# Optimization experiments

Measured on AMD Instinct MI355X. Metric: run time of the kernel, lower is better.

The kernel has to match this reference:

```python
import jax, jax.numpy as jnp
import numpy as np

LRELU_ALPHA = 0.2       # LeakyReLU slope (alpha arg of GraphAttentionLayer)
NEG_INF = -9e15         # zero_vec value from the torch code
N1, N2, N3 = 3000, 2500, 2500
IN_F, OUT_F, HEADS = 128, 64, 2


def setup_inputs() -> dict:
    key = jax.random.key(0)
    ks = jax.random.split(key, 13)
    N = N1 + N2 + N3
    h = jax.random.normal(ks[0], (N, IN_F), jnp.float32)
    A1  = jax.random.randint(ks[1],  (N1, N1), 0, 2, jnp.int32)
    A2  = jax.random.randint(ks[2],  (N2, N2), 0, 2, jnp.int32)
    A3  = jax.random.randint(ks[3],  (N3, N3), 0, 2, jnp.int32)
    A12 = jax.random.randint(ks[4],  (N1, N2), 0, 2, jnp.int32)
    A13 = jax.random.randint(ks[5],  (N1, N3), 0, 2, jnp.int32)
    A23 = jax.random.randint(ks[6],  (N2, N3), 0, 2, jnp.int32)
    A21 = jax.random.randint(ks[7],  (N2, N1), 0, 2, jnp.int32)
    A31 = jax.random.randint(ks[8],  (N3, N1), 0, 2, jnp.int32)
    A32 = jax.random.randint(ks[9],  (N3, N2), 0, 2, jnp.int32)
    # per-head GAT parameters (xavier-ish scale)
    Ws = jax.random.normal(ks[10], (HEADS, IN_F, OUT_F), jnp.float32) * 0.12
    a_param = jax.random.normal(ks[11], (HEADS, 2 * OUT_F, 1), jnp.float32) * 0.12
    return dict(h=h, A1=A1, A2=A2, A3=A3, A12=A12, A13=A13, A23=A23,
                A21=A21, A31=A31, A32=A32, Ws=Ws, a_param=a_param)


def reference(h, A1, A2, A3, A12, A13, A23, A21, A31, A32, Ws, a_param):
    n1, n2, n3 = A1.shape[0], A2.shape[0], A3.shape[0]
    # The 9 block assignments in the torch forward tile the full NxN matrix,
    # so they are equivalent to one block-structured mask.
    mask = jnp.block([[A1,  A12, A13],
                      [A21, A2,  A23],
                      [A31, A32, A3]]) > 0          # [N, N] bool

    Wh = jnp.einsum('nf,hfo->hno', h, Ws)           # [H, N, O]
    a1 = a_param[:, :OUT_F, 0]                      # [H, O]
    a2 = a_param[:, OUT_F:, 0]                      # [H, O]
    Wh1 = jnp.einsum('hno,ho->hn', Wh, a1)          # [H, N]
    Wh2 = jnp.einsum('hno,ho->hn', Wh, a2)          # [H, N]
    e = jax.nn.leaky_relu(Wh1[:, :, None] + Wh2[:, None, :], LRELU_ALPHA)  # [H,N,N]
    att = jax.nn.softmax(jnp.where(mask[None], e, NEG_INF), axis=-1)
    # dropout is identity in eval mode
    mid = jnp.einsum('hij,hjo->hio', att, Wh)       # [H, N, O]
    out = jax.nn.elu(mid)                           # concat=True -> elu
    x2 = out.transpose(1, 0, 2).reshape(h.shape[0], -1)  # [N, H*O] head concat

    x3 = jax.nn.log_softmax(x2[n1 + n2:], axis=1)   # group-3 nodes
    x4 = jax.nn.log_softmax(x2[:n1], axis=1)        # group-1 nodes
    x5 = jax.nn.log_softmax(x2[n1:n1 + n2], axis=1) # group-2 nodes
    return (x3, x4, x5)
```

## Files before the change

### kernel.cpp

```cpp
#include <hip/hip_runtime.h>
#include <hip/hip_bf16.h>


#define CN1 3000
#define CN2 2500
#define CN3 2500
#define NTOT 8000
#define INF_ 128
#define OUTF 64
#define LOG2E 1.44269504088896340736f
#define ALPHA 0.2f

typedef __attribute__((ext_vector_type(4))) float f32x4;
typedef __attribute__((ext_vector_type(8))) short short8;
union B16x8 { int4 i4; short8 s8; unsigned int u[4]; };

#if defined(__has_builtin)
#if __has_builtin(__builtin_amdgcn_exp2f)
#define EXP2F(x) __builtin_amdgcn_exp2f(x)
#endif
#endif
#ifndef EXP2F
#define EXP2F(x) exp2f(x)
#endif

__device__ inline float wave_sum(float v) {
  for (int d = 32; d; d >>= 1) v += __shfl_xor(v, d, 64);
  return v;
}

__device__ inline unsigned int pack2_bf16(float a, float b) {
  unsigned ua = __float_as_uint(a);
  ua = (ua + 0x7FFFu + ((ua >> 16) & 1u)) >> 16;
  unsigned ub = __float_as_uint(b);
  ub = (ub + 0x7FFFu + ((ub >> 16) & 1u)) & 0xFFFF0000u;
  return ub | ua;
}

__global__ void k_wh(const float* __restrict__ hv, const float* __restrict__ Wsv,
                     const float* __restrict__ ap,
                     float* __restrict__ Whf,
                     float* __restrict__ Wh1s,
                     float* __restrict__ Wh2s) {
  const int t = threadIdx.x;
  const int o = t & 63;
  const int n = blockIdx.x * 2 + (t >> 6);
  const float* hrow = hv + n * INF_;
  const float* Ws0 = Wsv + o;
  const float* Ws1 = Wsv + INF_ * OUTF + o;
  float a0a = 0.f, a0b = 0.f, a1a = 0.f, a1b = 0.f;
#pragma unroll 8
  for (int f = 0; f < INF_; f += 2) {
    float h0 = hrow[f], h1 = hrow[f + 1];
    a0a += h0 * Ws0[f * OUTF];
    a0b += h1 * Ws0[(f + 1) * OUTF];
    a1a += h0 * Ws1[f * OUTF];
    a1b += h1 * Ws1[(f + 1) * OUTF];
  }
  float acc0 = a0a + a0b, acc1 = a1a + a1b;
  Whf[(0 * NTOT + n) * OUTF + o] = acc0;
  Whf[(1 * NTOT + n) * OUTF + o] = acc1;
  float s10 = wave_sum(acc0 * ap[o]);
  float s20 = wave_sum(acc0 * ap[OUTF + o]);
  float s11 = wave_sum(acc1 * ap[2 * OUTF + o]);
  float s21 = wave_sum(acc1 * ap[3 * OUTF + o]);
  if (o == 0) {
    Wh1s[n] = s10 * LOG2E;        Wh2s[n] = s20 * LOG2E;
    Wh1s[NTOT + n] = s11 * LOG2E; Wh2s[NTOT + n] = s21 * LOG2E;
  }
}

__global__ void k_m2(const float* __restrict__ Wh2s, float* __restrict__ M2s) {
  const int hd = blockIdx.x;
  float mx = -1e30f;
  for (int i = threadIdx.x; i < NTOT; i += 256)
    mx = fmaxf(mx, Wh2s[hd * NTOT + i]);
  for (int d = 32; d; d >>= 1) mx = fmaxf(mx, __shfl_xor(mx, d, 64));
  __shared__ float red[4];
  if ((threadIdx.x & 63) == 0) red[threadIdx.x >> 6] = mx;
  __syncthreads();
  if (threadIdx.x == 0)
    M2s[hd] = fmaxf(fmaxf(red[0], red[1]), fmaxf(red[2], red[3]));
}

__global__ void k_bpack(const float* __restrict__ Whf, int4* __restrict__ WhB) {
  const int gid = blockIdx.x * 256 + threadIdx.x;
  const int lane = gid & 63;
  const int c = (gid >> 6) & 3;
  const int t = (gid >> 8) % 250;
  const int hd = gid / 64000;
  const int jb = t * 32 + (lane >> 4) * 8;
  const int col = c * 16 + (lane & 15);
  const float* src = Whf + (hd * NTOT + jb) * OUTF + col;
  B16x8 out;
#pragma unroll
  for (int e2 = 0; e2 < 4; ++e2)
    out.u[e2] = pack2_bf16(src[(2 * e2) * OUTF], src[(2 * e2 + 1) * OUTF]);
  WhB[gid] = out.i4;
}

__global__ __launch_bounds__(128, 2)
void k_attn_mfma(const int* __restrict__ A1,  const int* __restrict__ A12, const int* __restrict__ A13,
                 const int* __restrict__ A21, const int* __restrict__ A2,  const int* __restrict__ A23,
                 const int* __restrict__ A31, const int* __restrict__ A32, const int* __restrict__ A3,
                 const float* __restrict__ Wh1s, const float* __restrict__ Wh2s,
                 const float* __restrict__ M2s, const int4* __restrict__ WhB,
                 float* __restrict__ partAcc,
                 float* __restrict__ partS)
{
  const int widx = threadIdx.x >> 6;
  const int lane = threadIdx.x & 63;
  const int m = lane & 15;
  const int g = lane >> 4;
  const int kb = g * 8;
  const int rowblk = blockIdx.x * 2 + widx;
  const int i = rowblk * 16 + m;
  const int jy = blockIdx.y, njy = gridDim.y;
  const int t0 = (250 * jy) / njy, t1 = (250 * (jy + 1)) / njy;

  const int *p0, *p1, *p2;
  if (i < CN1)            { p0 = A1  + i * CN1;          p1 = A12 + i * CN2;          p2 = A13 + i * CN3; }
  else if (i < CN1 + CN2) { int r = i - CN1;       p0 = A21 + r * CN1; p1 = A2  + r * CN2; p2 = A23 + r * CN3; }
  else                    { int r = i - CN1 - CN2; p0 = A31 + r * CN1; p1 = A32 + r * CN2; p2 = A3  + r * CN3; }

  const float w1s0 = Wh1s[i],        w1s1 = Wh1s[NTOT + i];
  const float y0 = w1s0 + M2s[0],    y1 = w1s1 + M2s[1];
  const float ci0 = fmaxf(y0, ALPHA * y0), ci1 = fmaxf(y1, ALPHA * y1);
  const float a1c0 = w1s0 - ci0, b1c0 = ALPHA * w1s0 - ci0;
  const float a1c1 = w1s1 - ci1, b1c1 = ALPHA * w1s1 - ci1;
  const float* wh2_0 = Wh2s;
  const float* wh2_1 = Wh2s + NTOT;

  f32x4 a0_0 = {0.f,0.f,0.f,0.f}, a0_1 = a0_0, a0_2 = a0_0, a0_3 = a0_0;
  f32x4 a1_0 = a0_0, a1_1 = a0_0, a1_2 = a0_0, a1_3 = a0_0;
  float sp0 = 0.f, sp1 = 0.f;

  auto load_mask = [&](int t, int4& ma, int4& mb) {
    int j8 = t * 32 + kb;
    if (j8 >= CN1 + CN2) {
      const int4* q = (const int4*)(p2 + (j8 - CN1 - CN2));
      ma = q[0]; mb = q[1];
    } else if (j8 >= CN1) {
      if (j8 + 8 <= CN1 + CN2) {
        const int4* q = (const int4*)(p1 + (j8 - CN1));
        ma = q[0]; mb = q[1];
      } else {
        int v[8];
#pragma unroll
        for (int e = 0; e < 8; ++e) {
          int je = j8 + e;
          v[e] = (je < CN1 + CN2) ? p1[je - CN1] : p2[je - CN1 - CN2];
        }
        ma = make_int4(v[0], v[1], v[2], v[3]);
        mb = make_int4(v[4], v[5], v[6], v[7]);
      }
    } else {
      const int4* q = (const int4*)(p0 + j8);
      ma = q[0]; mb = q[1];
    }
  };

  struct Frags { int4 f0[4], f1[4]; float4 w0a, w0b, w1a, w1b; };
  auto load_frags = [&](int t, Frags& F) {
    const int4* bp0 = WhB + t * 256 + lane;
    const int4* bp1 = WhB + (250 + t) * 256 + lane;
#pragma unroll
    for (int c = 0; c < 4; ++c) { F.f0[c] = bp0[c * 64]; F.f1[c] = bp1[c * 64]; }
    const float* w0 = wh2_0 + t * 32 + kb;
    const float* w1 = wh2_1 + t * 32 + kb;
    F.w0a = *(const float4*)w0; F.w0b = *(const float4*)(w0 + 4);
    F.w1a = *(const float4*)w1; F.w1b = *(const float4*)(w1 + 4);
  };

  auto compute = [&](const int4& ma, const int4& mb, const Frags& F) {
    const int   mv[8] = {ma.x, ma.y, ma.z, ma.w, mb.x, mb.y, mb.z, mb.w};
    const float w0v[8] = {F.w0a.x, F.w0a.y, F.w0a.z, F.w0a.w, F.w0b.x, F.w0b.y, F.w0b.z, F.w0b.w};
    const float w1v[8] = {F.w1a.x, F.w1a.y, F.w1a.z, F.w1a.w, F.w1b.x, F.w1b.y, F.w1b.z, F.w1b.w};
    float q0[8], q1[8];
#pragma unroll
    for (int e = 0; e < 8; ++e) {
      bool on = (mv[e] > 0);
      float xa0 = a1c0 + w0v[e];
      float xb0 = fmaf(ALPHA, w0v[e], b1c0);
      float p0e = EXP2F(fmaxf(xa0, xb0));
      q0[e] = on ? p0e : 0.f;
      float xa1 = a1c1 + w1v[e];
      float xb1 = fmaf(ALPHA, w1v[e], b1c1);
      float p1e = EXP2F(fmaxf(xa1, xb1));
      q1[e] = on ? p1e : 0.f;
    }
    sp0 += ((q0[0] + q0[1]) + (q0[2] + q0[3])) + ((q0[4] + q0[5]) + (q0[6] + q0[7]));
    sp1 += ((q1[0] + q1[1]) + (q1[2] + q1[3])) + ((q1[4] + q1[5]) + (q1[6] + q1[7]));
    B16x8 af0, af1;
#pragma unroll
    for (int e2 = 0; e2 < 4; ++e2) {
      af0.u[e2] = pack2_bf16(q0[2 * e2], q0[2 * e2 + 1]);
      af1.u[e2] = pack2_bf16(q1[2 * e2], q1[2 * e2 + 1]);
    }
    B16x8 b;
    b.i4 = F.f0[0]; a0_0 = __builtin_amdgcn_mfma_f32_16x16x32_bf16(af0.s8, b.s8, a0_0, 0, 0, 0);
    b.i4 = F.f0[1]; a0_1 = __builtin_amdgcn_mfma_f32_16x16x32_bf16(af0.s8, b.s8, a0_1, 0, 0, 0);
    b.i4 = F.f0[2]; a0_2 = __builtin_amdgcn_mfma_f32_16x16x32_bf16(af0.s8, b.s8, a0_2, 0, 0, 0);
    b.i4 = F.f0[3]; a0_3 = __builtin_amdgcn_mfma_f32_16x16x32_bf16(af0.s8, b.s8, a0_3, 0, 0, 0);
    b.i4 = F.f1[0]; a1_0 = __builtin_amdgcn_mfma_f32_16x16x32_bf16(af1.s8, b.s8, a1_0, 0, 0, 0);
    b.i4 = F.f1[1]; a1_1 = __builtin_amdgcn_mfma_f32_16x16x32_bf16(af1.s8, b.s8, a1_1, 0, 0, 0);
    b.i4 = F.f1[2]; a1_2 = __builtin_amdgcn_mfma_f32_16x16x32_bf16(af1.s8, b.s8, a1_2, 0, 0, 0);
    b.i4 = F.f1[3]; a1_3 = __builtin_amdgcn_mfma_f32_16x16x32_bf16(af1.s8, b.s8, a1_3, 0, 0, 0);
  };

  int4 ma0, mb0, ma1, mb1, ma2, mb2, ma3, mb3;
  Frags Fc, Fn;
  load_mask(t0, ma0, mb0);
  load_mask(min(t0 + 1, t1 - 1), ma1, mb1);
  load_mask(min(t0 + 2, t1 - 1), ma2, mb2);
  load_frags(t0, Fc);
  for (int t = t0; t < t1; ++t) {
    load_frags(min(t + 1, t1 - 1), Fn);
    load_mask(min(t + 3, t1 - 1), ma3, mb3);
    compute(ma0, mb0, Fc);
    ma0 = ma1; mb0 = mb1; ma1 = ma2; mb1 = mb2; ma2 = ma3; mb2 = mb3;
    Fc = Fn;
  }

  sp0 += __shfl_xor(sp0, 16, 64); sp0 += __shfl_xor(sp0, 32, 64);
  sp1 += __shfl_xor(sp1, 16, 64); sp1 += __shfl_xor(sp1, 32, 64);
  const int base0 = (jy * 2 + 0) * NTOT + rowblk * 16;
  const int base1 = (jy * 2 + 1) * NTOT + rowblk * 16;
  if (lane < 16) {
    partS[base0 + lane] = sp0;
    partS[base1 + lane] = sp1;
  }

  float* o0 = partAcc + base0 * OUTF;
  float* o1 = partAcc + base1 * OUTF;
#pragma unroll
  for (int q = 0; q < 4; ++q) {
    const int row = g * 4 + q;
    o0[row * OUTF +      m] = a0_0[q];
    o0[row * OUTF + 16 + m] = a0_1[q];
    o0[row * OUTF + 32 + m] = a0_2[q];
    o0[row * OUTF + 48 + m] = a0_3[q];
    o1[row * OUTF +      m] = a1_0[q];
    o1[row * OUTF + 16 + m] = a1_1[q];
    o1[row * OUTF + 32 + m] = a1_2[q];
    o1[row * OUTF + 48 + m] = a1_3[q];
  }
}

__global__ void k_final(const float* __restrict__ partAcc, const float* __restrict__ partS,
                        int njy, float* __restrict__ out) {
  const int wave = threadIdx.x >> 6, lane = threadIdx.x & 63;
  const int n = blockIdx.x * 4 + wave;
  float x[2];
#pragma unroll
  for (int hd = 0; hd < 2; ++hd) {
    float a = 0.f, s = 0.f;
    for (int jy = 0; jy < njy; ++jy) {
      a += partAcc[((jy * 2 + hd) * NTOT + n) * OUTF + lane];
      s += partS[(jy * 2 + hd) * NTOT + n];
    }
    float mid = a / s;
    x[hd] = mid > 0.f ? mid : (__expf(mid) - 1.f);
  }
  float mx = fmaxf(x[0], x[1]);
  for (int d = 32; d; d >>= 1) mx = fmaxf(mx, __shfl_xor(mx, d, 64));
  float se = __expf(x[0] - mx) + __expf(x[1] - mx);
  for (int d = 32; d; d >>= 1) se += __shfl_xor(se, d, 64);
  const float lse = mx + __logf(se);
  const int orow = (n >= CN1 + CN2) ? (n - CN1 - CN2) : (n + CN3);
  out[orow * 128 + lane]      = x[0] - lse;
  out[orow * 128 + 64 + lane] = x[1] - lse;
}

__global__ void k_sentinel(float* __restrict__ out, float v) {
  out[blockIdx.x * 256 + threadIdx.x] = v;
}

extern "C" void kernel_launch(void* const* d_in, const int* in_sizes, int n_in,
                              void* d_out, int out_size, void* d_ws, size_t ws_size,
                              hipStream_t stream) {
  float* outf = (float*)d_out;

  static const int EXP[12] = {1024000, 9000000, 6250000, 6250000, 7500000, 7500000,
                              6250000, 7500000, 7500000, 6250000, 16384, 256};
  bool exact = (n_in == 12);
  if (exact) for (int i = 0; i < 12; ++i) if (in_sizes[i] != EXP[i]) { exact = false; break; }

  const size_t FIXED = 64000 + 64000 + 256 + 2048000;
  int njy = 0;
  for (int cand = 4; cand >= 1; cand >>= 1) {
    size_t need = FIXED + (size_t)cand * 64000 +
                  ((size_t)(cand > 1 ? cand : 1)) * 4096000;
    if (ws_size >= need) { njy = cand; break; }
  }
  if (!exact || njy == 0) {
    k_sentinel<<<dim3(4000), dim3(256), 0, stream>>>(outf, -148.0f);
    return;
  }

  const float* h  = (const float*)d_in[0];
  const int* A1  = (const int*)d_in[1];
  const int* A2  = (const int*)d_in[2];
  const int* A3  = (const int*)d_in[3];
  const int* A12 = (const int*)d_in[4];
  const int* A13 = (const int*)d_in[5];
  const int* A23 = (const int*)d_in[6];
  const int* A21 = (const int*)d_in[7];
  const int* A31 = (const int*)d_in[8];
  const int* A32 = (const int*)d_in[9];
  const float* Ws = (const float*)d_in[10];
  const float* ap = (const float*)d_in[11];

  char* w = (char*)d_ws;
  float* Wh1s    = (float*)(w);
  float* Wh2s    = (float*)(w + 64000);
  float* M2s     = (float*)(w + 128000);
  int4*  WhB     = (int4*) (w + 128256);
  float* partS   = (float*)(w + 2176256);
  float* Whf     = (float*)(w + 2176256 + (size_t)njy * 64000);
  float* partAcc = Whf;

  k_wh       <<<dim3(4000),     dim3(128), 0, stream>>>(h, Ws, ap, Whf, Wh1s, Wh2s);
  k_m2       <<<dim3(2),        dim3(256), 0, stream>>>(Wh2s, M2s);
  k_bpack    <<<dim3(500),      dim3(256), 0, stream>>>(Whf, WhB);
  k_attn_mfma<<<dim3(250, njy), dim3(128), 0, stream>>>(A1, A12, A13, A21, A2, A23, A31, A32, A3,
                                                        Wh1s, Wh2s, M2s, WhB, partAcc, partS);
  k_final    <<<dim3(2000),     dim3(256), 0, stream>>>(partAcc, partS, njy, outf);
}
```

Measured before the change: 407.9 us.

## Pre-pack adjacency masks into bitmasks before the attention MFMA kernel

```diff
diff --git a/kernel.cpp b/kernel.cpp
--- a/kernel.cpp
+++ b/kernel.cpp
@@ -35,6 +35,31 @@
   unsigned ub = __float_as_uint(b);
   ub = (ub + 0x7FFFu + ((ub >> 16) & 1u)) & 0xFFFF0000u;
   return ub | ua;
+}
+
+__global__ __launch_bounds__(256)
+void k_pack(const int* __restrict__ A1,  const int* __restrict__ A12, const int* __restrict__ A13,
+            const int* __restrict__ A21, const int* __restrict__ A2,  const int* __restrict__ A23,
+            const int* __restrict__ A31, const int* __restrict__ A32, const int* __restrict__ A3,
+            unsigned int* __restrict__ packed) {
+  const int i = blockIdx.x * 4 + (threadIdx.x >> 6);
+  const int lane = threadIdx.x & 63;
+  const int *p0, *p1, *p2;
+  if (i < CN1)            { p0 = A1  + i * CN1;          p1 = A12 + i * CN2;          p2 = A13 + i * CN3; }
+  else if (i < CN1 + CN2) { int r = i - CN1;       p0 = A21 + r * CN1; p1 = A2  + r * CN2; p2 = A23 + r * CN3; }
+  else                    { int r = i - CN1 - CN2; p0 = A31 + r * CN1; p1 = A32 + r * CN2; p2 = A3  + r * CN3; }
+  unsigned int* pkrow = packed + (i >> 4) * 4000 + (i & 15);
+  for (int c = 0; c < 125; ++c) {
+    const int j = c * 64 + lane;
+    int mval = (j < CN1) ? p0[j]
+             : (j < CN1 + CN2) ? p1[j - CN1]
+                               : p2[j - CN1 - CN2];
+    unsigned long long bm = __ballot(mval > 0);
+    if (lane == 0) {
+      pkrow[(2 * c) * 16]     = (unsigned int)(bm & 0xffffffffull);
+      pkrow[(2 * c + 1) * 16] = (unsigned int)(bm >> 32);
+    }
+  }
 }
 
 __global__ void k_wh(const float* __restrict__ hv, const float* __restrict__ Wsv,
@@ -100,9 +125,7 @@
 }
 
 __global__ __launch_bounds__(128, 2)
-void k_attn_mfma(const int* __restrict__ A1,  const int* __restrict__ A12, const int* __restrict__ A13,
-                 const int* __restrict__ A21, const int* __restrict__ A2,  const int* __restrict__ A23,
-                 const int* __restrict__ A31, const int* __restrict__ A32, const int* __restrict__ A3,
+void k_attn_mfma(const unsigned int* __restrict__ packed,
                  const float* __restrict__ Wh1s, const float* __restrict__ Wh2s,
                  const float* __restrict__ M2s, const int4* __restrict__ WhB,
                  float* __restrict__ partAcc,
@@ -118,10 +141,7 @@
   const int jy = blockIdx.y, njy = gridDim.y;
   const int t0 = (250 * jy) / njy, t1 = (250 * (jy + 1)) / njy;
 
-  const int *p0, *p1, *p2;
-  if (i < CN1)            { p0 = A1  + i * CN1;          p1 = A12 + i * CN2;          p2 = A13 + i * CN3; }
-  else if (i < CN1 + CN2) { int r = i - CN1;       p0 = A21 + r * CN1; p1 = A2  + r * CN2; p2 = A23 + r * CN3; }
-  else                    { int r = i - CN1 - CN2; p0 = A31 + r * CN1; p1 = A32 + r * CN2; p2 = A3  + r * CN3; }
+  const unsigned int* pkb = packed + rowblk * 4000 + m;
 
   const float w1s0 = Wh1s[i],        w1s1 = Wh1s[NTOT + i];
   const float y0 = w1s0 + M2s[0],    y1 = w1s1 + M2s[1];
@@ -135,31 +155,6 @@
   f32x4 a1_0 = a0_0, a1_1 = a0_0, a1_2 = a0_0, a1_3 = a0_0;
   float sp0 = 0.f, sp1 = 0.f;
 
-  auto load_mask = [&](int t, int4& ma, int4& mb) {
-    int j8 = t * 32 + kb;
-    if (j8 >= CN1 + CN2) {
-      const int4* q = (const int4*)(p2 + (j8 - CN1 - CN2));
-      ma = q[0]; mb = q[1];
-    } else if (j8 >= CN1) {
-      if (j8 + 8 <= CN1 + CN2) {
-        const int4* q = (const int4*)(p1 + (j8 - CN1));
-        ma = q[0]; mb = q[1];
-      } else {
-        int v[8];
-#pragma unroll
-        for (int e = 0; e < 8; ++e) {
-          int je = j8 + e;
-          v[e] = (je < CN1 + CN2) ? p1[je - CN1] : p2[je - CN1 - CN2];
-        }
-        ma = make_int4(v[0], v[1], v[2], v[3]);
-        mb = make_int4(v[4], v[5], v[6], v[7]);
-      }
-    } else {
-      const int4* q = (const int4*)(p0 + j8);
-      ma = q[0]; mb = q[1];
-    }
-  };
-
   struct Frags { int4 f0[4], f1[4]; float4 w0a, w0b, w1a, w1b; };
   auto load_frags = [&](int t, Frags& F) {
     const int4* bp0 = WhB + t * 256 + lane;
@@ -172,14 +167,14 @@
     F.w1a = *(const float4*)w1; F.w1b = *(const float4*)(w1 + 4);
   };
 
-  auto compute = [&](const int4& ma, const int4& mb, const Frags& F) {
-    const int   mv[8] = {ma.x, ma.y, ma.z, ma.w, mb.x, mb.y, mb.z, mb.w};
+  auto compute = [&](unsigned int mw, const Frags& F) {
+    const unsigned bits = (mw >> kb) & 0xffu;
     const float w0v[8] = {F.w0a.x, F.w0a.y, F.w0a.z, F.w0a.w, F.w0b.x, F.w0b.y, F.w0b.z, F.w0b.w};
     const float w1v[8] = {F.w1a.x, F.w1a.y, F.w1a.z, F.w1a.w, F.w1b.x, F.w1b.y, F.w1b.z, F.w1b.w};
     float q0[8], q1[8];
 #pragma unroll
     for (int e = 0; e < 8; ++e) {
-      bool on = (mv[e] > 0);
+      bool on = ((bits >> e) & 1u) != 0u;
       float xa0 = a1c0 + w0v[e];
       float xb0 = fmaf(ALPHA, w0v[e], b1c0);
       float p0e = EXP2F(fmaxf(xa0, xb0));
@@ -208,17 +203,15 @@
     b.i4 = F.f1[3]; a1_3 = __builtin_amdgcn_mfma_f32_16x16x32_bf16(af1.s8, b.s8, a1_3, 0, 0, 0);
   };
 
-  int4 ma0, mb0, ma1, mb1, ma2, mb2, ma3, mb3;
+  unsigned int mw0 = pkb[t0 * 16];
+  unsigned int mw1 = pkb[min(t0 + 1, t1 - 1) * 16];
   Frags Fc, Fn;
-  load_mask(t0, ma0, mb0);
-  load_mask(min(t0 + 1, t1 - 1), ma1, mb1);
-  load_mask(min(t0 + 2, t1 - 1), ma2, mb2);
   load_frags(t0, Fc);
   for (int t = t0; t < t1; ++t) {
     load_frags(min(t + 1, t1 - 1), Fn);
-    load_mask(min(t + 3, t1 - 1), ma3, mb3);
-    compute(ma0, mb0, Fc);
-    ma0 = ma1; mb0 = mb1; ma1 = ma2; mb1 = mb2; ma2 = ma3; mb2 = mb3;
+    unsigned int mw2 = pkb[min(t + 2, t1 - 1) * 16];
+    compute(mw0, Fc);
+    mw0 = mw1; mw1 = mw2;
     Fc = Fn;
   }
 
@@ -286,11 +279,10 @@
   bool exact = (n_in == 12);
   if (exact) for (int i = 0; i < 12; ++i) if (in_sizes[i] != EXP[i]) { exact = false; break; }
 
-  const size_t FIXED = 64000 + 64000 + 256 + 2048000;
+  const size_t FIXED = 64000 + 64000 + 256 + 2048000 + 8000000;
   int njy = 0;
   for (int cand = 4; cand >= 1; cand >>= 1) {
-    size_t need = FIXED + (size_t)cand * 64000 +
-                  ((size_t)(cand > 1 ? cand : 1)) * 4096000;
+    size_t need = FIXED + (size_t)cand * 64000 + (size_t)cand * 4096000;
     if (ws_size >= need) { njy = cand; break; }
   }
   if (!exact || njy == 0) {
@@ -312,18 +304,21 @@
   const float* ap = (const float*)d_in[11];
 
   char* w = (char*)d_ws;
-  float* Wh1s    = (float*)(w);
-  float* Wh2s    = (float*)(w + 64000);
-  float* M2s     = (float*)(w + 128000);
-  int4*  WhB     = (int4*) (w + 128256);
-  float* partS   = (float*)(w + 2176256);
-  float* Whf     = (float*)(w + 2176256 + (size_t)njy * 64000);
-  float* partAcc = Whf;
-
+  float*        Wh1s    = (float*)(w);
+  float*        Wh2s    = (float*)(w + 64000);
+  float*        M2s     = (float*)(w + 128000);
+  int4*         WhB     = (int4*) (w + 128256);
+  unsigned int* packed  = (unsigned int*)(w + 2176256);
+  float*        partS   = (float*)(w + 10176256);
+  float*        Whf     = (float*)(w + 10176256 + (size_t)njy * 64000);
+  float*        partAcc = Whf;
+
+  k_pack     <<<dim3(2000),     dim3(256), 0, stream>>>(A1, A12, A13, A21, A2, A23, A31, A32, A3,
+                                                        packed);
   k_wh       <<<dim3(4000),     dim3(128), 0, stream>>>(h, Ws, ap, Whf, Wh1s, Wh2s);
   k_m2       <<<dim3(2),        dim3(256), 0, stream>>>(Wh2s, M2s);
   k_bpack    <<<dim3(500),      dim3(256), 0, stream>>>(Whf, WhB);
-  k_attn_mfma<<<dim3(250, njy), dim3(128), 0, stream>>>(A1, A12, A13, A21, A2, A23, A31, A32, A3,
-                                                        Wh1s, Wh2s, M2s, WhB, partAcc, partS);
+  k_attn_mfma<<<dim3(250, njy), dim3(128), 0, stream>>>(packed, Wh1s, Wh2s, M2s, WhB,
+                                                        partAcc, partS);
   k_final    <<<dim3(2000),     dim3(256), 0, stream>>>(partAcc, partS, njy, outf);
 }
```

Result: slower. 422.8 us (+3.7%).
